# Performance work log

Measured on AMD Instinct MI355X. Metric: run time of the kernel, lower is better.

## Reference

```python
import jax, jax.numpy as jnp
import numpy as np

N, H, E, T, ED, AB = 50000, 64, 800000, 800000, 64, 16


def setup_inputs() -> dict:
    key = jax.random.key(0)
    ks = jax.random.split(key, 26)

    def nrm(k, shape, scale=1.0):
        return jax.random.normal(k, shape, dtype=jnp.float32) * scale

    d = {}
    d["s"] = nrm(ks[0], (N, H))
    d["v"] = nrm(ks[1], (N, H, 3))
    d["edge_index"] = jax.random.randint(ks[2], (2, E), 0, N, dtype=jnp.int32)
    d["edge_rbf"] = jax.random.uniform(ks[3], (E, ED), dtype=jnp.float32)
    raw_dir = jax.random.normal(ks[4], (E, 3), dtype=jnp.float32)
    d["edge_dir"] = raw_dir / jnp.linalg.norm(raw_dir, axis=-1, keepdims=True)
    d["triplet_kj"] = jax.random.randint(ks[5], (T,), 0, E, dtype=jnp.int32)
    d["triplet_ji"] = jax.random.randint(ks[6], (T,), 0, E, dtype=jnp.int32)
    d["angle_feat"] = jax.random.uniform(ks[7], (T, AB), dtype=jnp.float32)

    def lin(kw, kb, fan_in, fan_out):
        sc = 1.0 / np.sqrt(fan_in)
        return nrm(kw, (fan_in, fan_out), sc), nrm(kb, (fan_out,), sc)

    d["W_t1"], d["b_t1"] = lin(ks[8], ks[9], 2 * ED + AB, H)
    d["W_t2"], d["b_t2"] = lin(ks[10], ks[11], H, H)
    d["W_m1"], d["b_m1"] = lin(ks[12], ks[13], 2 * H + ED + H, H)
    d["W_m2"], d["b_m2"] = lin(ks[14], ks[15], H, 2 * H)
    d["W_u1"], d["b_u1"] = lin(ks[16], ks[17], 3 * H, H)
    d["W_u2"], d["b_u2"] = lin(ks[18], ks[19], H, H)
    d["W_g1"], d["b_g1"] = lin(ks[20], ks[21], 3 * H, H)
    d["W_g2"], d["b_g2"] = lin(ks[22], ks[23], H, H)
    d["ln_g"] = jnp.ones((H,), jnp.float32)
    d["ln_b"] = jnp.zeros((H,), jnp.float32)
    return d


def _mlp(x, W1, b1, W2, b2):
    return jax.nn.silu(x @ W1 + b1) @ W2 + b2


def reference(s, v, edge_index, edge_rbf, edge_dir, triplet_kj, triplet_ji,
              angle_feat, W_t1, b_t1, W_t2, b_t2, W_m1, b_m1, W_m2, b_m2,
              W_u1, b_u1, W_u2, b_u2, W_g1, b_g1, W_g2, b_g2, ln_g, ln_b):
    n_nodes, hid = s.shape
    n_edges = edge_rbf.shape[0]

    # 3-body triplet messages: gather two edge rbf rows + angle feature
    t_in = jnp.concatenate([edge_rbf[triplet_kj], edge_rbf[triplet_ji], angle_feat], axis=-1)
    t_msg = _mlp(t_in, W_t1, b_t1, W_t2, b_t2)                 # [T, H]
    angle_agg = jax.ops.segment_sum(t_msg, triplet_ji, num_segments=n_edges)  # [E, H]

    src, dst = edge_index[0], edge_index[1]
    msg_in = jnp.concatenate([s[src], s[dst], edge_rbf, angle_agg], axis=-1)  # [E, 4H]
    msg = _mlp(msg_in, W_m1, b_m1, W_m2, b_m2)                 # [E, 2H]
    m_s, m_v_coeff = jnp.split(msg, 2, axis=-1)

    agg_s = jax.ops.segment_sum(m_s, dst, num_segments=n_nodes)  # [N, H]
    m_v = m_v_coeff[:, :, None] * edge_dir[:, None, :]          # [E, H, 3]
    agg_v = jax.ops.segment_sum(m_v.reshape(n_edges, hid * 3), dst,
                                num_segments=n_nodes).reshape(n_nodes, hid, 3)

    v_norm = jnp.linalg.norm(v, axis=-1)                        # [N, H]
    ctx = jnp.concatenate([s, agg_s, v_norm], axis=-1)          # [N, 3H]
    s_new = s + _mlp(ctx, W_u1, b_u1, W_u2, b_u2)
    gate = jax.nn.sigmoid(_mlp(ctx, W_g1, b_g1, W_g2, b_g2))
    v_new = v + gate[..., None] * agg_v

    mu = s_new.mean(axis=-1, keepdims=True)
    var = s_new.var(axis=-1, keepdims=True)
    s_ln = (s_new - mu) / jnp.sqrt(var + 1e-5) * ln_g + ln_b
    s_out = jax.nn.silu(s_ln)
    return (s_out, v_new)
```

## Files before the change

kernel.cpp:

```cpp
#include <hip/hip_runtime.h>
#include <cstdint>
#include <cstddef>

#define NN 50000
#define NE 800000
#define NT 800000

typedef unsigned short u16;
typedef unsigned int u32;
typedef __attribute__((ext_vector_type(8))) short short8;
typedef __attribute__((ext_vector_type(4))) float f32x4;

__device__ __forceinline__ float silu_f(float x) { return x / (1.f + __expf(-x)); }
__device__ __forceinline__ float sigm_f(float x) { return 1.f / (1.f + __expf(-x)); }
__device__ __forceinline__ u16 f2b(float x) {
  u32 u = __float_as_uint(x);
  u32 r = u + 0x7fffu + ((u >> 16) & 1u);
  return (u16)(r >> 16);
}
__device__ __forceinline__ float b2f(u16 h) { return __uint_as_float(((u32)h) << 16); }

template <int RW>
__device__ __forceinline__ int lx(int r, int c) {
  return r * RW + ((((c >> 3) ^ (r & 7)) << 3) | (c & 7));
}

__global__ __launch_bounds__(256) void kcvt2(const float* __restrict__ erbf,
                                             u16* __restrict__ erbf_bf,
                                             const float* __restrict__ s,
                                             u16* __restrict__ s_bf) {
  int i = blockIdx.x * 256 + threadIdx.x;
  const float* in;
  u16* out;
  int j;
  if (i < NE * 16) { in = erbf; out = erbf_bf; j = i; }
  else { j = i - NE * 16; if (j >= NN * 16) return; in = s; out = s_bf; }
  float4 v = ((const float4*)in)[j];
  uint2 p;
  p.x = (u32)f2b(v.x) | ((u32)f2b(v.y) << 16);
  p.y = (u32)f2b(v.z) | ((u32)f2b(v.w) << 16);
  ((uint2*)out)[j] = p;
}

__global__ __launch_bounds__(256) void khist2(const int* __restrict__ tji,
                                              const int* __restrict__ edst,
                                              int* __restrict__ tcnt,
                                              int* __restrict__ ncnt) {
  int i = blockIdx.x * 256 + threadIdx.x;
  if (i < NT) atomicAdd(&tcnt[tji[i]], 1);
  else {
    int j = i - NT;
    if (j < NE) atomicAdd(&ncnt[edst[j]], 1);
  }
}

__global__ __launch_bounds__(256) void kscan1b(
    const int* __restrict__ inA, int nA, int* __restrict__ outA, int* __restrict__ bsA, int BA,
    const int* __restrict__ inB, int nB, int* __restrict__ outB, int* __restrict__ bsB) {
  __shared__ int sh[256];
  const int* in; int n; int* out; int* bs; int blk;
  if ((int)blockIdx.x < BA) { in = inA; n = nA; out = outA; bs = bsA; blk = blockIdx.x; }
  else { in = inB; n = nB; out = outB; bs = bsB; blk = blockIdx.x - BA; }
  int tid = threadIdx.x;
  size_t base = (size_t)blk * 1024;
  int v[4];
  int acc = 0;
#pragma unroll
  for (int q = 0; q < 4; ++q) {
    size_t i = base + (size_t)tid * 4 + q;
    int x = (i < (size_t)n) ? in[i] : 0;
    v[q] = acc;
    acc += x;
  }
  sh[tid] = acc;
  __syncthreads();
  for (int off = 1; off < 256; off <<= 1) {
    int y = (tid >= off) ? sh[tid - off] : 0;
    __syncthreads();
    sh[tid] += y;
    __syncthreads();
  }
  int excl = (tid == 0) ? 0 : sh[tid - 1];
  if (tid == 255) bs[blk] = sh[255];
#pragma unroll
  for (int q = 0; q < 4; ++q) {
    size_t i = base + (size_t)tid * 4 + q;
    if (i < (size_t)n) out[i] = excl + v[q];
  }
}

__global__ __launch_bounds__(1024) void kscan2b(int* __restrict__ bsA, int nbA,
                                                int* __restrict__ bsB, int nbB) {
  __shared__ int sh[1024];
  int* bs = (blockIdx.x == 0) ? bsA : bsB;
  int nb = (blockIdx.x == 0) ? nbA : nbB;
  int tid = threadIdx.x;
  sh[tid] = (tid < nb) ? bs[tid] : 0;
  __syncthreads();
  for (int off = 1; off < 1024; off <<= 1) {
    int y = (tid >= off) ? sh[tid - off] : 0;
    __syncthreads();
    sh[tid] += y;
    __syncthreads();
  }
  if (tid < nb) bs[tid] = (tid == 0) ? 0 : sh[tid - 1];
}

__global__ __launch_bounds__(256) void kscan3b(
    int* __restrict__ outA, const int* __restrict__ bsA, int nA, int totalA,
    int* __restrict__ outB, const int* __restrict__ bsB, int nB, int totalB) {
  int i = blockIdx.x * 256 + threadIdx.x;
  if (i <= nA) {
    if (i < nA) outA[i] += bsA[i >> 10];
    else outA[nA] = totalA;
  } else {
    int j = i - (nA + 1);
    if (j < nB) outB[j] += bsB[j >> 10];
    else if (j == nB) outB[nB] = totalB;
  }
}

__global__ __launch_bounds__(256) void kscatter_inv_afeat(
    const int* __restrict__ keys, const int* __restrict__ off, int n,
    int* __restrict__ cnt, int* __restrict__ tids,
    const float* __restrict__ afeat, u16* __restrict__ afeat_s) {
  int i = blockIdx.x * 256 + threadIdx.x;
  if (i < n) {
    int k = keys[i];
    int slot = off[k] + (atomicSub(&cnt[k], 1) - 1);
    tids[slot] = i;
    const float4* src = (const float4*)(afeat + (size_t)i * 16);
    uint2* dst = (uint2*)(afeat_s + (size_t)slot * 16);
#pragma unroll
    for (int q = 0; q < 4; ++q) {
      float4 v = src[q];
      uint2 p;
      p.x = (u32)f2b(v.x) | ((u32)f2b(v.y) << 16);
      p.y = (u32)f2b(v.z) | ((u32)f2b(v.w) << 16);
      dst[q] = p;
    }
  }
}

__global__ __launch_bounds__(256) void kscatter_fwd_dir(const int* __restrict__ keys,
                                                        const int* __restrict__ off, int n,
                                                        int* __restrict__ cnt,
                                                        int* __restrict__ eids,
                                                        const float* __restrict__ dir,
                                                        float* __restrict__ dir_s) {
  int i = blockIdx.x * 256 + threadIdx.x;
  if (i < n) {
    int k = keys[i];
    int slot = off[k] + (atomicSub(&cnt[k], 1) - 1);
    eids[slot] = i;
    dir_s[(size_t)slot * 3 + 0] = dir[(size_t)i * 3 + 0];
    dir_s[(size_t)slot * 3 + 1] = dir[(size_t)i * 3 + 1];
    dir_s[(size_t)slot * 3 + 2] = dir[(size_t)i * 3 + 2];
  }
}

__global__ __launch_bounds__(256) void kprepw_all(
    const float* __restrict__ Wt1, const float* __restrict__ Wt2,
    const float* __restrict__ Wm1, const float* __restrict__ Wm2,
    const float* __restrict__ Wu1, const float* __restrict__ Wu2,
    const float* __restrict__ Wg1, const float* __restrict__ Wg2,
    u16* __restrict__ Pt1, u16* __restrict__ Pt2,
    u16* __restrict__ Pm1, u16* __restrict__ Pm2,
    u16* __restrict__ Pu1, u16* __restrict__ Pu2,
    u16* __restrict__ Pg1, u16* __restrict__ Pg2) {
  int gid = blockIdx.x * 256 + threadIdx.x;
  int f = gid >> 6, l = gid & 63;
  const float* W; u16* out; int K, N, fl;
  if (f < 20)       { W = Wt1; out = Pt1; K = 144; N = 64;  fl = f; }
  else if (f < 28)  { W = Wt2; out = Pt2; K = 64;  N = 64;  fl = f - 20; }
  else if (f < 60)  { W = Wm1; out = Pm1; K = 256; N = 64;  fl = f - 28; }
  else if (f < 76)  { W = Wm2; out = Pm2; K = 64;  N = 128; fl = f - 60; }
  else if (f < 100) { W = Wu1; out = Pu1; K = 192; N = 64;  fl = f - 76; }
  else if (f < 108) { W = Wu2; out = Pu2; K = 64;  N = 64;  fl = f - 100; }
  else if (f < 132) { W = Wg1; out = Pg1; K = 192; N = 64;  fl = f - 108; }
  else if (f < 140) { W = Wg2; out = Pg2; K = 64;  N = 64;  fl = f - 132; }
  else return;
  int nt = fl % (N / 16);
  int kt = fl / (N / 16);
  int k0 = kt * 32 + (l >> 4) * 8;
  int n = nt * 16 + (l & 15);
  u16 vals[8];
#pragma unroll
  for (int j = 0; j < 8; ++j) {
    int kk = k0 + j;
    vals[j] = (kk < K) ? f2b(W[(size_t)kk * N + n]) : (u16)0;
  }
  uint4* dst = (uint4*)(out + (size_t)fl * 512 + l * 8);
  uint4 p;
  p.x = (u32)vals[0] | ((u32)vals[1] << 16);
  p.y = (u32)vals[2] | ((u32)vals[3] << 16);
  p.z = (u32)vals[4] | ((u32)vals[5] << 16);
  p.w = (u32)vals[6] | ((u32)vals[7] << 16);
  *dst = p;
}

__global__ __launch_bounds__(256) void ktrip_mfma(
    const int* __restrict__ tkj, const int* __restrict__ tji,
    const u16* __restrict__ erbf_bf, const u16* __restrict__ afeat_s,
    const int* __restrict__ tids,
    const u16* __restrict__ Wp1, const float* __restrict__ b1,
    const u16* __restrict__ Wp2, const float* __restrict__ b2,
    u16* __restrict__ tmsg_s) {
  __shared__ u16 Xs[64 * 192];
  __shared__ u16 Hs[64 * 64];
  const int tid = threadIdx.x;
  const int l = tid & 63;
  const int w = tid >> 6;
  const int st0 = blockIdx.x * 64;

#pragma unroll
  for (int it = 0; it < 4; ++it) {
    int idx = it * 256 + tid;
    int sel = idx >> 9, r = (idx >> 3) & 63, ch = idx & 7;
    int t = tids[st0 + r];
    int node = sel ? tji[t] : tkj[t];
    uint4 vv = *(const uint4*)&erbf_bf[(size_t)node * 64 + ch * 8];
    *(uint4*)&Xs[lx<192>(r, sel * 64 + ch * 8)] = vv;
  }
  {
    int r = tid >> 2, c = (tid & 3) * 4;
    uint2 p2 = *(const uint2*)&afeat_s[(size_t)(st0 + r) * 16 + c];
    *(uint2*)&Xs[lx<192>(r, 128 + c)] = p2;
  }
#pragma unroll
  for (int i = 0; i < 2; ++i) {
    int idx = i * 256 + tid;
    int r = idx >> 3, c = 144 + (idx & 7) * 2;
    *(u32*)&Xs[lx<192>(r, c)] = 0;
  }
  __syncthreads();

  f32x4 acc1[4];
  {
    float bias = b1[w * 16 + (l & 15)];
#pragma unroll
    for (int mt = 0; mt < 4; ++mt) acc1[mt] = (f32x4){bias, bias, bias, bias};
    for (int ks = 0; ks < 5; ++ks) {
      short8 bf = *(const short8*)(Wp1 + ((size_t)(ks * 4 + w) * 64 + l) * 8);
#pragma unroll
      for (int mt = 0; mt < 4; ++mt) {
        short8 af = *(const short8*)&Xs[lx<192>(mt * 16 + (l & 15), ks * 32 + ((l >> 4) << 3))];
        acc1[mt] = __builtin_amdgcn_mfma_f32_16x16x32_bf16(af, bf, acc1[mt], 0, 0, 0);
      }
    }
  }
#pragma unroll
  for (int mt = 0; mt < 4; ++mt)
#pragma unroll
    for (int q = 0; q < 4; ++q) {
      int r = mt * 16 + (l >> 4) * 4 + q;
      Hs[lx<64>(r, w * 16 + (l & 15))] = f2b(silu_f(acc1[mt][q]));
    }
  __syncthreads();

  f32x4 acc2[4];
  {
    float bias = b2[w * 16 + (l & 15)];
#pragma unroll
    for (int mt = 0; mt < 4; ++mt) acc2[mt] = (f32x4){bias, bias, bias, bias};
    for (int ks = 0; ks < 2; ++ks) {
      short8 bf = *(const short8*)(Wp2 + ((size_t)(ks * 4 + w) * 64 + l) * 8);
#pragma unroll
      for (int mt = 0; mt < 4; ++mt) {
        short8 af = *(const short8*)&Hs[lx<64>(mt * 16 + (l & 15), ks * 32 + ((l >> 4) << 3))];
        acc2[mt] = __builtin_amdgcn_mfma_f32_16x16x32_bf16(af, bf, acc2[mt], 0, 0, 0);
      }
    }
  }
  __syncthreads();
#pragma unroll
  for (int mt = 0; mt < 4; ++mt)
#pragma unroll
    for (int q = 0; q < 4; ++q) {
      int r = mt * 16 + (l >> 4) * 4 + q;
      Xs[lx<64>(r, w * 16 + (l & 15))] = f2b(acc2[mt][q]);
    }
  __syncthreads();
  for (int i = 0; i < 2; ++i) {
    int idx = i * 256 + tid;
    int r = idx >> 3, c0 = (idx & 7) << 3;
    uint4 val = *(const uint4*)&Xs[lx<64>(r, c0)];
    *(uint4*)(tmsg_s + (size_t)(st0 + r) * 64 + c0) = val;
  }
}

__global__ __launch_bounds__(256) void kmsg_mfma(
    const int* __restrict__ eidx, const u16* __restrict__ s_bf,
    const u16* __restrict__ erbf_bf,
    const int* __restrict__ toff, const u16* __restrict__ tmsg_s,
    const int* __restrict__ eids,
    const u16* __restrict__ Wp1, const float* __restrict__ b1,
    const u16* __restrict__ Wp2, const float* __restrict__ b2,
    u16* __restrict__ msg_s) {
  __shared__ u16 Xs[64 * 256];
  __shared__ u16 Hs[64 * 64];
  const int tid = threadIdx.x;
  const int l = tid & 63;
  const int w = tid >> 6;
  const int sl0 = blockIdx.x * 64;

#pragma unroll
  for (int i = 0; i < 2; ++i) {
    int idx = i * 256 + tid;
    int r = idx >> 3, c0 = (idx & 7) << 3;
    int e = eids[sl0 + r];
    uint4 vv = *(const uint4*)&erbf_bf[(size_t)e * 64 + c0];
    *(uint4*)&Xs[lx<256>(r, 128 + c0)] = vv;
  }
#pragma unroll
  for (int it = 0; it < 4; ++it) {
    int idx = it * 256 + tid;
    int sel = idx >> 9, r = (idx >> 3) & 63, ch = idx & 7;
    int e = eids[sl0 + r];
    int node = eidx[sel * NE + e];
    uint4 vv = *(const uint4*)&s_bf[(size_t)node * 64 + ch * 8];
    *(uint4*)&Xs[lx<256>(r, sel * 64 + ch * 8)] = vv;
  }
#pragma unroll
  for (int it = 0; it < 2; ++it) {
    int idx = it * 256 + tid;
    int r = idx >> 3, ch = idx & 7;
    int e = eids[sl0 + r];
    int r0 = toff[e], r1 = toff[e + 1];
    float a[8];
#pragma unroll
    for (int j = 0; j < 8; ++j) a[j] = 0.f;
    for (int ri = r0; ri < r1; ++ri) {
      uint4 pk = *(const uint4*)&tmsg_s[(size_t)ri * 64 + ch * 8];
      a[0] += b2f((u16)(pk.x & 0xffff)); a[1] += b2f((u16)(pk.x >> 16));
      a[2] += b2f((u16)(pk.y & 0xffff)); a[3] += b2f((u16)(pk.y >> 16));
      a[4] += b2f((u16)(pk.z & 0xffff)); a[5] += b2f((u16)(pk.z >> 16));
      a[6] += b2f((u16)(pk.w & 0xffff)); a[7] += b2f((u16)(pk.w >> 16));
    }
    uint4 p;
    p.x = (u32)f2b(a[0]) | ((u32)f2b(a[1]) << 16);
    p.y = (u32)f2b(a[2]) | ((u32)f2b(a[3]) << 16);
    p.z = (u32)f2b(a[4]) | ((u32)f2b(a[5]) << 16);
    p.w = (u32)f2b(a[6]) | ((u32)f2b(a[7]) << 16);
    *(uint4*)&Xs[lx<256>(r, 192 + ch * 8)] = p;
  }
  __syncthreads();

  f32x4 acc1[4];
  {
    float bias = b1[w * 16 + (l & 15)];
#pragma unroll
    for (int mt = 0; mt < 4; ++mt) acc1[mt] = (f32x4){bias, bias, bias, bias};
    for (int ks = 0; ks < 8; ++ks) {
      short8 bf = *(const short8*)(Wp1 + ((size_t)(ks * 4 + w) * 64 + l) * 8);
#pragma unroll
      for (int mt = 0; mt < 4; ++mt) {
        short8 af = *(const short8*)&Xs[lx<256>(mt * 16 + (l & 15), ks * 32 + ((l >> 4) << 3))];
        acc1[mt] = __builtin_amdgcn_mfma_f32_16x16x32_bf16(af, bf, acc1[mt], 0, 0, 0);
      }
    }
  }
#pragma unroll
  for (int mt = 0; mt < 4; ++mt)
#pragma unroll
    for (int q = 0; q < 4; ++q) {
      int r = mt * 16 + (l >> 4) * 4 + q;
      Hs[lx<64>(r, w * 16 + (l & 15))] = f2b(silu_f(acc1[mt][q]));
    }
  __syncthreads();

  f32x4 acc2[2][4];
#pragma unroll
  for (int pp = 0; pp < 2; ++pp) {
    int nt = w * 2 + pp;
    float bias = b2[nt * 16 + (l & 15)];
#pragma unroll
    for (int mt = 0; mt < 4; ++mt) acc2[pp][mt] = (f32x4){bias, bias, bias, bias};
    for (int ks = 0; ks < 2; ++ks) {
      short8 bf = *(const short8*)(Wp2 + ((size_t)(ks * 8 + nt) * 64 + l) * 8);
#pragma unroll
      for (int mt = 0; mt < 4; ++mt) {
        short8 af = *(const short8*)&Hs[lx<64>(mt * 16 + (l & 15), ks * 32 + ((l >> 4) << 3))];
        acc2[pp][mt] = __builtin_amdgcn_mfma_f32_16x16x32_bf16(af, bf, acc2[pp][mt], 0, 0, 0);
      }
    }
  }
  __syncthreads();
#pragma unroll
  for (int pp = 0; pp < 2; ++pp)
#pragma unroll
    for (int mt = 0; mt < 4; ++mt)
#pragma unroll
      for (int q = 0; q < 4; ++q) {
        int r = mt * 16 + (l >> 4) * 4 + q;
        Xs[lx<128>(r, (w * 2 + pp) * 16 + (l & 15))] = f2b(acc2[pp][mt][q]);
      }
  __syncthreads();
  for (int i = 0; i < 4; ++i) {
    int idx = i * 256 + tid;
    int r = idx >> 4, c0 = (idx & 15) << 3;
    uint4 val = *(const uint4*)&Xs[lx<128>(r, c0)];
    *(uint4*)(msg_s + (size_t)(sl0 + r) * 128 + c0) = val;
  }
}

__global__ __launch_bounds__(256) void kagg(
    const int* __restrict__ noff, const u16* __restrict__ msg_s,
    const float* __restrict__ dir_s,
    u16* __restrict__ aggs_bf, float* __restrict__ aggv) {
  const int lane = threadIdx.x & 63;
  const int wv = threadIdx.x >> 6;
  const int n = blockIdx.x * 4 + wv;
  if (n >= NN) return;
  const int r0 = noff[n], r1 = noff[n + 1];
  const int lrow = lane >> 4, lcol = lane & 15;
  const bool is_ms = (lcol < 8);

  float a[8];
  float v0[8], v1[8], v2[8];
#pragma unroll
  for (int j = 0; j < 8; ++j) { a[j] = 0.f; v0[j] = 0.f; v1[j] = 0.f; v2[j] = 0.f; }

  for (int r4 = r0; r4 < r1; r4 += 4) {
    int r = r4 + lrow;
    if (r < r1) {
      uint4 pk = *(const uint4*)&msg_s[(size_t)r * 128 + lcol * 8];
      float x[8];
      x[0] = b2f((u16)(pk.x & 0xffff)); x[1] = b2f((u16)(pk.x >> 16));
      x[2] = b2f((u16)(pk.y & 0xffff)); x[3] = b2f((u16)(pk.y >> 16));
      x[4] = b2f((u16)(pk.z & 0xffff)); x[5] = b2f((u16)(pk.z >> 16));
      x[6] = b2f((u16)(pk.w & 0xffff)); x[7] = b2f((u16)(pk.w >> 16));
      if (is_ms) {
#pragma unroll
        for (int j = 0; j < 8; ++j) a[j] += x[j];
      } else {
        float dx = dir_s[(size_t)r * 3 + 0];
        float dy = dir_s[(size_t)r * 3 + 1];
        float dz = dir_s[(size_t)r * 3 + 2];
#pragma unroll
        for (int j = 0; j < 8; ++j) {
          v0[j] += x[j] * dx; v1[j] += x[j] * dy; v2[j] += x[j] * dz;
        }
      }
    }
  }
#pragma unroll
  for (int j = 0; j < 8; ++j) {
    a[j] += __shfl_xor(a[j], 16);  a[j] += __shfl_xor(a[j], 32);
    v0[j] += __shfl_xor(v0[j], 16); v0[j] += __shfl_xor(v0[j], 32);
    v1[j] += __shfl_xor(v1[j], 16); v1[j] += __shfl_xor(v1[j], 32);
    v2[j] += __shfl_xor(v2[j], 16); v2[j] += __shfl_xor(v2[j], 32);
  }
  if (lrow == 0) {
    if (is_ms) {
      uint4 p;
      p.x = (u32)f2b(a[0]) | ((u32)f2b(a[1]) << 16);
      p.y = (u32)f2b(a[2]) | ((u32)f2b(a[3]) << 16);
      p.z = (u32)f2b(a[4]) | ((u32)f2b(a[5]) << 16);
      p.w = (u32)f2b(a[6]) | ((u32)f2b(a[7]) << 16);
      *(uint4*)&aggs_bf[(size_t)n * 64 + lcol * 8] = p;
    } else {
      int c0 = (lcol - 8) * 8;
      float* av = aggv + (size_t)n * 192 + (size_t)c0 * 3;
      float4 o0 = {v0[0], v1[0], v2[0], v0[1]};
      float4 o1 = {v1[1], v2[1], v0[2], v1[2]};
      float4 o2 = {v2[2], v0[3], v1[3], v2[3]};
      float4 o3 = {v0[4], v1[4], v2[4], v0[5]};
      float4 o4 = {v1[5], v2[5], v0[6], v1[6]};
      float4 o5 = {v2[6], v0[7], v1[7], v2[7]};
      float4* av4 = (float4*)av;
      av4[0] = o0; av4[1] = o1; av4[2] = o2; av4[3] = o3; av4[4] = o4; av4[5] = o5;
    }
  }
}

__global__ __launch_bounds__(256) void knode_mfma(
    const u16* __restrict__ s_bf, const float* __restrict__ v,
    const u16* __restrict__ aggs_bf, const float* __restrict__ aggv,
    const u16* __restrict__ WpU1, const float* __restrict__ bU1,
    const u16* __restrict__ WpU2, const float* __restrict__ bU2,
    const u16* __restrict__ WpG1, const float* __restrict__ bG1,
    const u16* __restrict__ WpG2, const float* __restrict__ bG2,
    const float* __restrict__ lng, const float* __restrict__ lnb,
    float* __restrict__ outs, float* __restrict__ outv) {
  __shared__ __align__(16) char smem[64 * 192 * 2 + 2 * 64 * 64 * 2];
  u16* Xs = (u16*)smem;
  u16* Hu = (u16*)(smem + 64 * 192 * 2);
  u16* Hg = Hu + 64 * 64;
  float* Fs = (float*)smem;

  const int tid = threadIdx.x;
  const int l = tid & 63;
  const int w = tid >> 6;
  const int n0 = blockIdx.x * 64;

  for (int i = 0; i < 2; ++i) {
    int idx = i * 256 + tid;
    int r = idx >> 3, c0 = (idx & 7) << 3;
    int nr = n0 + r; if (nr >= NN) nr = NN - 1;
    uint4 a = *(const uint4*)&s_bf[(size_t)nr * 64 + c0];
    *(uint4*)&Xs[lx<192>(r, c0)] = a;
    uint4 b = *(const uint4*)&aggs_bf[(size_t)nr * 64 + c0];
    *(uint4*)&Xs[lx<192>(r, 64 + c0)] = b;
  }
  for (int it = 0; it < 16; ++it) {
    int idx = it * 256 + tid;
    int r = idx >> 6, c = idx & 63;
    int nr = n0 + r; if (nr >= NN) nr = NN - 1;
    const float* vp = v + (size_t)nr * 192 + c * 3;
    float x = vp[0], y = vp[1], z = vp[2];
    Xs[lx<192>(r, 128 + c)] = f2b(sqrtf(x * x + y * y + z * z));
  }
  __syncthreads();

  f32x4 au[4], ag[4];
  {
    float biu = bU1[w * 16 + (l & 15)], big = bG1[w * 16 + (l & 15)];
#pragma unroll
    for (int mt = 0; mt < 4; ++mt) {
      au[mt] = (f32x4){biu, biu, biu, biu};
      ag[mt] = (f32x4){big, big, big, big};
    }
    for (int ks = 0; ks < 6; ++ks) {
      short8 bu = *(const short8*)(WpU1 + ((size_t)(ks * 4 + w) * 64 + l) * 8);
      short8 bg = *(const short8*)(WpG1 + ((size_t)(ks * 4 + w) * 64 + l) * 8);
#pragma unroll
      for (int mt = 0; mt < 4; ++mt) {
        short8 af = *(const short8*)&Xs[lx<192>(mt * 16 + (l & 15), ks * 32 + ((l >> 4) << 3))];
        au[mt] = __builtin_amdgcn_mfma_f32_16x16x32_bf16(af, bu, au[mt], 0, 0, 0);
        ag[mt] = __builtin_amdgcn_mfma_f32_16x16x32_bf16(af, bg, ag[mt], 0, 0, 0);
      }
    }
  }
#pragma unroll
  for (int mt = 0; mt < 4; ++mt)
#pragma unroll
    for (int q = 0; q < 4; ++q) {
      int r = mt * 16 + (l >> 4) * 4 + q;
      Hu[lx<64>(r, w * 16 + (l & 15))] = f2b(silu_f(au[mt][q]));
      Hg[lx<64>(r, w * 16 + (l & 15))] = f2b(silu_f(ag[mt][q]));
    }
  __syncthreads();

  f32x4 ou[4], og[4];
  {
    float biu = bU2[w * 16 + (l & 15)], big = bG2[w * 16 + (l & 15)];
#pragma unroll
    for (int mt = 0; mt < 4; ++mt) {
      ou[mt] = (f32x4){biu, biu, biu, biu};
      og[mt] = (f32x4){big, big, big, big};
    }
    for (int ks = 0; ks < 2; ++ks) {
      short8 bu = *(const short8*)(WpU2 + ((size_t)(ks * 4 + w) * 64 + l) * 8);
      short8 bg = *(const short8*)(WpG2 + ((size_t)(ks * 4 + w) * 64 + l) * 8);
#pragma unroll
      for (int mt = 0; mt < 4; ++mt) {
        short8 afu = *(const short8*)&Hu[lx<64>(mt * 16 + (l & 15), ks * 32 + ((l >> 4) << 3))];
        ou[mt] = __builtin_amdgcn_mfma_f32_16x16x32_bf16(afu, bu, ou[mt], 0, 0, 0);
        short8 afg = *(const short8*)&Hg[lx<64>(mt * 16 + (l & 15), ks * 32 + ((l >> 4) << 3))];
        og[mt] = __builtin_amdgcn_mfma_f32_16x16x32_bf16(afg, bg, og[mt], 0, 0, 0);
      }
    }
  }
#pragma unroll
  for (int mt = 0; mt < 4; ++mt)
#pragma unroll
    for (int q = 0; q < 4; ++q) {
      int r = mt * 16 + (l >> 4) * 4 + q;
      ou[mt][q] += b2f(Xs[lx<192>(r, w * 16 + (l & 15))]);
    }
  __syncthreads();

#pragma unroll
  for (int mt = 0; mt < 4; ++mt)
#pragma unroll
    for (int q = 0; q < 4; ++q) {
      int r = mt * 16 + (l >> 4) * 4 + q;
      Fs[r * 68 + w * 16 + (l & 15)] = ou[mt][q];
    }
  __syncthreads();
  {
    int r = tid >> 2, c0 = (tid & 3) * 16;
    float xv[16];
#pragma unroll
    for (int j4 = 0; j4 < 4; ++j4) {
      float4 t = *(const float4*)&Fs[r * 68 + c0 + j4 * 4];
      xv[j4 * 4 + 0] = t.x; xv[j4 * 4 + 1] = t.y;
      xv[j4 * 4 + 2] = t.z; xv[j4 * 4 + 3] = t.w;
    }
    float sm = 0.f, sq = 0.f;
#pragma unroll
    for (int j = 0; j < 16; ++j) { sm += xv[j]; sq += xv[j] * xv[j]; }
    sm += __shfl_xor(sm, 1); sq += __shfl_xor(sq, 1);
    sm += __shfl_xor(sm, 2); sq += __shfl_xor(sq, 2);
    float mu = sm * (1.f / 64.f);
    float var = sq * (1.f / 64.f) - mu * mu;
    float rstd = rsqrtf(var + 1e-5f);
    if (n0 + r < NN) {
      float* op = outs + (size_t)(n0 + r) * 64 + c0;
#pragma unroll
      for (int j4 = 0; j4 < 4; ++j4) {
        float4 o;
        float y0 = (xv[j4 * 4 + 0] - mu) * rstd * lng[c0 + j4 * 4 + 0] + lnb[c0 + j4 * 4 + 0];
        float y1 = (xv[j4 * 4 + 1] - mu) * rstd * lng[c0 + j4 * 4 + 1] + lnb[c0 + j4 * 4 + 1];
        float y2 = (xv[j4 * 4 + 2] - mu) * rstd * lng[c0 + j4 * 4 + 2] + lnb[c0 + j4 * 4 + 2];
        float y3 = (xv[j4 * 4 + 3] - mu) * rstd * lng[c0 + j4 * 4 + 3] + lnb[c0 + j4 * 4 + 3];
        o.x = silu_f(y0); o.y = silu_f(y1); o.z = silu_f(y2); o.w = silu_f(y3);
        *(float4*)(op + j4 * 4) = o;
      }
    }
  }
  __syncthreads();

#pragma unroll
  for (int mt = 0; mt < 4; ++mt)
#pragma unroll
    for (int q = 0; q < 4; ++q) {
      int r = mt * 16 + (l >> 4) * 4 + q;
      Fs[r * 68 + w * 16 + (l & 15)] = og[mt][q];
    }
  __syncthreads();
  {
    int r = tid >> 2, c0 = (tid & 3) * 16;
    int nr = n0 + r;
    if (nr < NN) {
      float gate[16];
#pragma unroll
      for (int j = 0; j < 16; ++j) gate[j] = sigm_f(Fs[r * 68 + c0 + j]);
      const float4* vp = (const float4*)(v + (size_t)nr * 192 + c0 * 3);
      const float4* ap = (const float4*)(aggv + (size_t)nr * 192 + c0 * 3);
      float4* op = (float4*)(outv + (size_t)nr * 192 + c0 * 3);
#pragma unroll
      for (int j4 = 0; j4 < 12; ++j4) {
        float4 vv = vp[j4], av = ap[j4], o;
        o.x = vv.x + gate[(j4 * 4 + 0) / 3] * av.x;
        o.y = vv.y + gate[(j4 * 4 + 1) / 3] * av.y;
        o.z = vv.z + gate[(j4 * 4 + 2) / 3] * av.z;
        o.w = vv.w + gate[(j4 * 4 + 3) / 3] * av.w;
        op[j4] = o;
      }
    }
  }
}

extern "C" void kernel_launch(void* const* d_in, const int* in_sizes, int n_in,
                              void* d_out, int out_size, void* d_ws, size_t ws_size,
                              hipStream_t stream) {
  const float* s     = (const float*)d_in[0];
  const float* v     = (const float*)d_in[1];
  const int*   eidx  = (const int*)d_in[2];
  const float* erbf  = (const float*)d_in[3];
  const float* edir  = (const float*)d_in[4];
  const int*   tkj   = (const int*)d_in[5];
  const int*   tji   = (const int*)d_in[6];
  const float* afeat = (const float*)d_in[7];
  const float* W_t1  = (const float*)d_in[8];
  const float* b_t1  = (const float*)d_in[9];
  const float* W_t2  = (const float*)d_in[10];
  const float* b_t2  = (const float*)d_in[11];
  const float* W_m1  = (const float*)d_in[12];
  const float* b_m1  = (const float*)d_in[13];
  const float* W_m2  = (const float*)d_in[14];
  const float* b_m2  = (const float*)d_in[15];
  const float* W_u1  = (const float*)d_in[16];
  const float* b_u1  = (const float*)d_in[17];
  const float* W_u2  = (const float*)d_in[18];
  const float* b_u2  = (const float*)d_in[19];
  const float* W_g1  = (const float*)d_in[20];
  const float* b_g1  = (const float*)d_in[21];
  const float* W_g2  = (const float*)d_in[22];
  const float* b_g2  = (const float*)d_in[23];
  const float* ln_g  = (const float*)d_in[24];
  const float* ln_b  = (const float*)d_in[25];

  char* w = (char*)d_ws;
  auto alloc = [&](size_t bytes) -> char* {
    char* p = w;
    w += (bytes + 255) & ~(size_t)255;
    return p;
  };
  int* toff  = (int*)alloc((size_t)(NE + 1) * 4);
  int* noff  = (int*)alloc((size_t)(NN + 1) * 4);
  int* tcnt  = (int*)alloc((size_t)NE * 4);
  int* ncnt  = (int*)alloc((size_t)NN * 4);
  int* tids  = (int*)alloc((size_t)NT * 4);
  int* eids  = (int*)alloc((size_t)NE * 4);
  int* bsum  = (int*)alloc(2048 * 4);
  float* dir_s = (float*)alloc((size_t)NE * 3 * 4);
  u16* msg_s  = (u16*)alloc((size_t)NE * 128 * 2);
  u16* tmsg_s = (u16*)alloc((size_t)NT * 64 * 2);
  u16* erbf_bf = (u16*)alloc((size_t)NE * 64 * 2);
  u16* s_bf    = (u16*)alloc((size_t)NN * 64 * 2);
  u16* Wp_t1 = (u16*)alloc((size_t)5 * 4 * 512 * 2);
  u16* Wp_t2 = (u16*)alloc((size_t)2 * 4 * 512 * 2);
  u16* Wp_m1 = (u16*)alloc((size_t)8 * 4 * 512 * 2);
  u16* Wp_m2 = (u16*)alloc((size_t)2 * 8 * 512 * 2);
  u16* Wp_u1 = (u16*)alloc((size_t)6 * 4 * 512 * 2);
  u16* Wp_u2 = (u16*)alloc((size_t)2 * 4 * 512 * 2);
  u16* Wp_g1 = (u16*)alloc((size_t)6 * 4 * 512 * 2);
  u16* Wp_g2 = (u16*)alloc((size_t)2 * 4 * 512 * 2);
  u16* afeat_s = msg_s;
  float* aggv = (float*)tmsg_s;
  u16* aggs_bf = tmsg_s + (size_t)NN * 384;

  hipMemsetAsync(tcnt, 0, (size_t)((char*)(ncnt + NN) - (char*)tcnt), stream);

  kcvt2<<<(NE * 16 + NN * 16 + 255) / 256, 256, 0, stream>>>(erbf, erbf_bf, s, s_bf);
  khist2<<<(NT + NE + 255) / 256, 256, 0, stream>>>(tji, eidx + NE, tcnt, ncnt);

  const int Bt = (NE + 1023) / 1024, Bn = (NN + 1023) / 1024;
  kscan1b<<<Bt + Bn, 256, 0, stream>>>(tcnt, NE, toff, bsum, Bt, ncnt, NN, noff, bsum + 1024);
  kscan2b<<<2, 1024, 0, stream>>>(bsum, Bt, bsum + 1024, Bn);
  kscan3b<<<(NE + 1 + NN + 1 + 255) / 256, 256, 0, stream>>>(toff, bsum, NE, NT,
                                                             noff, bsum + 1024, NN, NE);

  kscatter_inv_afeat<<<(NT + 255) / 256, 256, 0, stream>>>(tji, toff, NT, tcnt, tids,
                                                           afeat, afeat_s);
  kscatter_fwd_dir<<<(NE + 255) / 256, 256, 0, stream>>>(eidx + NE, noff, NE, ncnt, eids,
                                                         edir, dir_s);

  kprepw_all<<<35, 256, 0, stream>>>(W_t1, W_t2, W_m1, W_m2, W_u1, W_u2, W_g1, W_g2,
                                     Wp_t1, Wp_t2, Wp_m1, Wp_m2, Wp_u1, Wp_u2, Wp_g1, Wp_g2);

  ktrip_mfma<<<NT / 64, 256, 0, stream>>>(tkj, tji, erbf_bf, afeat_s, tids,
                                          Wp_t1, b_t1, Wp_t2, b_t2, tmsg_s);
  kmsg_mfma<<<NE / 64, 256, 0, stream>>>(eidx, s_bf, erbf_bf, toff, tmsg_s, eids,
                                         Wp_m1, b_m1, Wp_m2, b_m2, msg_s);
  kagg<<<(NN + 3) / 4, 256, 0, stream>>>(noff, msg_s, dir_s, aggs_bf, aggv);

  float* out_s = (float*)d_out;
  float* out_v = out_s + (size_t)NN * 64;
  knode_mfma<<<(NN + 63) / 64, 256, 0, stream>>>(s_bf, v, aggs_bf, aggv,
                                                 Wp_u1, b_u1, Wp_u2, b_u2,
                                                 Wp_g1, b_g1, Wp_g2, b_g2,
                                                 ln_g, ln_b, out_s, out_v);
}
```

Measured before the change: 643.5 us.

## Fuse node aggregation into message kernel epilogue and merge prep kernels

The per-node aggregation kernel is removed. The edge message MLP kernel now reduces its 64 dst-sorted rows in its epilogue, writing directly for segments contained in the tile and using float atomics for segments that cross tile boundaries. This avoids writing and re-reading the bf16 msg_s buffer of 800k by 128 values. The three prep kernels (two scatters and the weight packing) are merged into one launch, and the fp32 aggregation buffers are now zeroed by the memset. In exchange the epilogue runs a serial 64-row loop on only 128 threads, and atomic contention on boundary nodes makes the accumulation order nondeterministic.

```diff
diff --git a/kernel.cpp b/kernel.cpp
--- a/kernel.cpp
+++ b/kernel.cpp
@@ -19,6 +19,9 @@
   return (u16)(r >> 16);
 }
 __device__ __forceinline__ float b2f(u16 h) { return __uint_as_float(((u32)h) << 16); }
+__device__ __forceinline__ u32 pk2(float a, float b) {
+  return (u32)f2b(a) | ((u32)f2b(b) << 16);
+}
 
 template <int RW>
 __device__ __forceinline__ int lx(int r, int c) {
@@ -37,8 +40,8 @@
   else { j = i - NE * 16; if (j >= NN * 16) return; in = s; out = s_bf; }
   float4 v = ((const float4*)in)[j];
   uint2 p;
-  p.x = (u32)f2b(v.x) | ((u32)f2b(v.y) << 16);
-  p.y = (u32)f2b(v.z) | ((u32)f2b(v.w) << 16);
+  p.x = pk2(v.x, v.y);
+  p.y = pk2(v.z, v.w);
   ((uint2*)out)[j] = p;
 }
 
@@ -120,46 +123,11 @@
   }
 }
 
-__global__ __launch_bounds__(256) void kscatter_inv_afeat(
-    const int* __restrict__ keys, const int* __restrict__ off, int n,
-    int* __restrict__ cnt, int* __restrict__ tids,
-    const float* __restrict__ afeat, u16* __restrict__ afeat_s) {
-  int i = blockIdx.x * 256 + threadIdx.x;
-  if (i < n) {
-    int k = keys[i];
-    int slot = off[k] + (atomicSub(&cnt[k], 1) - 1);
-    tids[slot] = i;
-    const float4* src = (const float4*)(afeat + (size_t)i * 16);
-    uint2* dst = (uint2*)(afeat_s + (size_t)slot * 16);
-#pragma unroll
-    for (int q = 0; q < 4; ++q) {
-      float4 v = src[q];
-      uint2 p;
-      p.x = (u32)f2b(v.x) | ((u32)f2b(v.y) << 16);
-      p.y = (u32)f2b(v.z) | ((u32)f2b(v.w) << 16);
-      dst[q] = p;
-    }
-  }
-}
-
-__global__ __launch_bounds__(256) void kscatter_fwd_dir(const int* __restrict__ keys,
-                                                        const int* __restrict__ off, int n,
-                                                        int* __restrict__ cnt,
-                                                        int* __restrict__ eids,
-                                                        const float* __restrict__ dir,
-                                                        float* __restrict__ dir_s) {
-  int i = blockIdx.x * 256 + threadIdx.x;
-  if (i < n) {
-    int k = keys[i];
-    int slot = off[k] + (atomicSub(&cnt[k], 1) - 1);
-    eids[slot] = i;
-    dir_s[(size_t)slot * 3 + 0] = dir[(size_t)i * 3 + 0];
-    dir_s[(size_t)slot * 3 + 1] = dir[(size_t)i * 3 + 1];
-    dir_s[(size_t)slot * 3 + 2] = dir[(size_t)i * 3 + 2];
-  }
-}
-
-__global__ __launch_bounds__(256) void kprepw_all(
+__global__ __launch_bounds__(256) void kprep_all(
+    const int* __restrict__ tji, const int* __restrict__ toff, int* __restrict__ tcnt,
+    int* __restrict__ tids, const float* __restrict__ afeat, u16* __restrict__ afeat_s,
+    const int* __restrict__ edst, const int* __restrict__ noff, int* __restrict__ ncnt,
+    int* __restrict__ eids, const float* __restrict__ dir, float* __restrict__ dir_s,
     const float* __restrict__ Wt1, const float* __restrict__ Wt2,
     const float* __restrict__ Wm1, const float* __restrict__ Wm2,
     const float* __restrict__ Wu1, const float* __restrict__ Wu2,
@@ -168,35 +136,60 @@
     u16* __restrict__ Pm1, u16* __restrict__ Pm2,
     u16* __restrict__ Pu1, u16* __restrict__ Pu2,
     u16* __restrict__ Pg1, u16* __restrict__ Pg2) {
-  int gid = blockIdx.x * 256 + threadIdx.x;
-  int f = gid >> 6, l = gid & 63;
-  const float* W; u16* out; int K, N, fl;
-  if (f < 20)       { W = Wt1; out = Pt1; K = 144; N = 64;  fl = f; }
-  else if (f < 28)  { W = Wt2; out = Pt2; K = 64;  N = 64;  fl = f - 20; }
-  else if (f < 60)  { W = Wm1; out = Pm1; K = 256; N = 64;  fl = f - 28; }
-  else if (f < 76)  { W = Wm2; out = Pm2; K = 64;  N = 128; fl = f - 60; }
-  else if (f < 100) { W = Wu1; out = Pu1; K = 192; N = 64;  fl = f - 76; }
-  else if (f < 108) { W = Wu2; out = Pu2; K = 64;  N = 64;  fl = f - 100; }
-  else if (f < 132) { W = Wg1; out = Pg1; K = 192; N = 64;  fl = f - 108; }
-  else if (f < 140) { W = Wg2; out = Pg2; K = 64;  N = 64;  fl = f - 132; }
-  else return;
-  int nt = fl % (N / 16);
-  int kt = fl / (N / 16);
-  int k0 = kt * 32 + (l >> 4) * 8;
-  int n = nt * 16 + (l & 15);
-  u16 vals[8];
-#pragma unroll
-  for (int j = 0; j < 8; ++j) {
-    int kk = k0 + j;
-    vals[j] = (kk < K) ? f2b(W[(size_t)kk * N + n]) : (u16)0;
-  }
-  uint4* dst = (uint4*)(out + (size_t)fl * 512 + l * 8);
-  uint4 p;
-  p.x = (u32)vals[0] | ((u32)vals[1] << 16);
-  p.y = (u32)vals[2] | ((u32)vals[3] << 16);
-  p.z = (u32)vals[4] | ((u32)vals[5] << 16);
-  p.w = (u32)vals[6] | ((u32)vals[7] << 16);
-  *dst = p;
+  int i = blockIdx.x * 256 + threadIdx.x;
+  if (i < NT) {
+    int k = tji[i];
+    int slot = toff[k] + (atomicSub(&tcnt[k], 1) - 1);
+    tids[slot] = i;
+    const float4* src = (const float4*)(afeat + (size_t)i * 16);
+    uint2* dst = (uint2*)(afeat_s + (size_t)slot * 16);
+#pragma unroll
+    for (int q = 0; q < 4; ++q) {
+      float4 v = src[q];
+      uint2 p;
+      p.x = pk2(v.x, v.y);
+      p.y = pk2(v.z, v.w);
+      dst[q] = p;
+    }
+  } else if (i < NT + NE) {
+    int j = i - NT;
+    int k = edst[j];
+    int slot = noff[k] + (atomicSub(&ncnt[k], 1) - 1);
+    eids[slot] = j;
+    dir_s[(size_t)slot * 3 + 0] = dir[(size_t)j * 3 + 0];
+    dir_s[(size_t)slot * 3 + 1] = dir[(size_t)j * 3 + 1];
+    dir_s[(size_t)slot * 3 + 2] = dir[(size_t)j * 3 + 2];
+  } else {
+    int g = i - NT - NE;
+    int f = g >> 6, l = g & 63;
+    const float* W; u16* out; int K, N, fl;
+    if (f < 20)       { W = Wt1; out = Pt1; K = 144; N = 64;  fl = f; }
+    else if (f < 28)  { W = Wt2; out = Pt2; K = 64;  N = 64;  fl = f - 20; }
+    else if (f < 60)  { W = Wm1; out = Pm1; K = 256; N = 64;  fl = f - 28; }
+    else if (f < 76)  { W = Wm2; out = Pm2; K = 64;  N = 128; fl = f - 60; }
+    else if (f < 100) { W = Wu1; out = Pu1; K = 192; N = 64;  fl = f - 76; }
+    else if (f < 108) { W = Wu2; out = Pu2; K = 64;  N = 64;  fl = f - 100; }
+    else if (f < 132) { W = Wg1; out = Pg1; K = 192; N = 64;  fl = f - 108; }
+    else if (f < 140) { W = Wg2; out = Pg2; K = 64;  N = 64;  fl = f - 132; }
+    else return;
+    int nt = fl % (N / 16);
+    int kt = fl / (N / 16);
+    int k0 = kt * 32 + (l >> 4) * 8;
+    int n = nt * 16 + (l & 15);
+    u16 vals[8];
+#pragma unroll
+    for (int j = 0; j < 8; ++j) {
+      int kk = k0 + j;
+      vals[j] = (kk < K) ? f2b(W[(size_t)kk * N + n]) : (u16)0;
+    }
+    uint4* dst = (uint4*)(out + (size_t)fl * 512 + l * 8);
+    uint4 p;
+    p.x = (u32)vals[0] | ((u32)vals[1] << 16);
+    p.y = (u32)vals[2] | ((u32)vals[3] << 16);
+    p.z = (u32)vals[4] | ((u32)vals[5] << 16);
+    p.w = (u32)vals[6] | ((u32)vals[7] << 16);
+    *dst = p;
+  }
 }
 
 __global__ __launch_bounds__(256) void ktrip_mfma(
@@ -293,12 +286,16 @@
     const int* __restrict__ eidx, const u16* __restrict__ s_bf,
     const u16* __restrict__ erbf_bf,
     const int* __restrict__ toff, const u16* __restrict__ tmsg_s,
-    const int* __restrict__ eids,
+    const int* __restrict__ eids, const int* __restrict__ noff,
+    const float* __restrict__ dir_s,
     const u16* __restrict__ Wp1, const float* __restrict__ b1,
     const u16* __restrict__ Wp2, const float* __restrict__ b2,
-    u16* __restrict__ msg_s) {
-  __shared__ u16 Xs[64 * 256];
-  __shared__ u16 Hs[64 * 64];
+    float* __restrict__ aggs_f, float* __restrict__ aggv) {
+  __shared__ __align__(16) char smemM[64 * 256 * 2 + 64 * 64 * 2];
+  u16* Xs = (u16*)smemM;
+  u16* Hs = (u16*)(smemM + 64 * 256 * 2);
+  int* dstL = (int*)(smemM + 64 * 256 * 2);
+  float* dirL = (float*)(smemM + 64 * 256 * 2 + 256);
   const int tid = threadIdx.x;
   const int l = tid & 63;
   const int w = tid >> 6;
@@ -338,10 +335,10 @@
       a[6] += b2f((u16)(pk.w & 0xffff)); a[7] += b2f((u16)(pk.w >> 16));
     }
     uint4 p;
-    p.x = (u32)f2b(a[0]) | ((u32)f2b(a[1]) << 16);
-    p.y = (u32)f2b(a[2]) | ((u32)f2b(a[3]) << 16);
-    p.z = (u32)f2b(a[4]) | ((u32)f2b(a[5]) << 16);
-    p.w = (u32)f2b(a[6]) | ((u32)f2b(a[7]) << 16);
+    p.x = pk2(a[0], a[1]);
+    p.y = pk2(a[2], a[3]);
+    p.z = pk2(a[4], a[5]);
+    p.w = pk2(a[6], a[7]);
     *(uint4*)&Xs[lx<256>(r, 192 + ch * 8)] = p;
   }
   __syncthreads();
@@ -386,6 +383,7 @@
     }
   }
   __syncthreads();
+
 #pragma unroll
   for (int pp = 0; pp < 2; ++pp)
 #pragma unroll
@@ -395,88 +393,58 @@
         int r = mt * 16 + (l >> 4) * 4 + q;
         Xs[lx<128>(r, (w * 2 + pp) * 16 + (l & 15))] = f2b(acc2[pp][mt][q]);
       }
-  __syncthreads();
-  for (int i = 0; i < 4; ++i) {
-    int idx = i * 256 + tid;
-    int r = idx >> 4, c0 = (idx & 15) << 3;
-    uint4 val = *(const uint4*)&Xs[lx<128>(r, c0)];
-    *(uint4*)(msg_s + (size_t)(sl0 + r) * 128 + c0) = val;
-  }
-}
-
-__global__ __launch_bounds__(256) void kagg(
-    const int* __restrict__ noff, const u16* __restrict__ msg_s,
-    const float* __restrict__ dir_s,
-    u16* __restrict__ aggs_bf, float* __restrict__ aggv) {
-  const int lane = threadIdx.x & 63;
-  const int wv = threadIdx.x >> 6;
-  const int n = blockIdx.x * 4 + wv;
-  if (n >= NN) return;
-  const int r0 = noff[n], r1 = noff[n + 1];
-  const int lrow = lane >> 4, lcol = lane & 15;
-  const bool is_ms = (lcol < 8);
-
-  float a[8];
-  float v0[8], v1[8], v2[8];
-#pragma unroll
-  for (int j = 0; j < 8; ++j) { a[j] = 0.f; v0[j] = 0.f; v1[j] = 0.f; v2[j] = 0.f; }
-
-  for (int r4 = r0; r4 < r1; r4 += 4) {
-    int r = r4 + lrow;
-    if (r < r1) {
-      uint4 pk = *(const uint4*)&msg_s[(size_t)r * 128 + lcol * 8];
-      float x[8];
-      x[0] = b2f((u16)(pk.x & 0xffff)); x[1] = b2f((u16)(pk.x >> 16));
-      x[2] = b2f((u16)(pk.y & 0xffff)); x[3] = b2f((u16)(pk.y >> 16));
-      x[4] = b2f((u16)(pk.z & 0xffff)); x[5] = b2f((u16)(pk.z >> 16));
-      x[6] = b2f((u16)(pk.w & 0xffff)); x[7] = b2f((u16)(pk.w >> 16));
-      if (is_ms) {
-#pragma unroll
-        for (int j = 0; j < 8; ++j) a[j] += x[j];
-      } else {
-        float dx = dir_s[(size_t)r * 3 + 0];
-        float dy = dir_s[(size_t)r * 3 + 1];
-        float dz = dir_s[(size_t)r * 3 + 2];
-#pragma unroll
-        for (int j = 0; j < 8; ++j) {
-          v0[j] += x[j] * dx; v1[j] += x[j] * dy; v2[j] += x[j] * dz;
+  if (tid < 64) {
+    int e = eids[sl0 + tid];
+    dstL[tid] = eidx[NE + e];
+    dirL[tid * 3 + 0] = dir_s[(size_t)(sl0 + tid) * 3 + 0];
+    dirL[tid * 3 + 1] = dir_s[(size_t)(sl0 + tid) * 3 + 1];
+    dirL[tid * 3 + 2] = dir_s[(size_t)(sl0 + tid) * 3 + 2];
+  }
+  __syncthreads();
+
+  if (tid < 128) {
+    const int j = tid;
+    const bool ms = (j < 64);
+    float a0 = 0.f, a1 = 0.f, a2 = 0.f;
+    int cur = dstL[0];
+    for (int r = 0; r < 64; ++r) {
+      int d = dstL[r];
+      if (d != cur) {
+        bool interior = (noff[cur] >= sl0) && (noff[cur + 1] <= sl0 + 64);
+        if (ms) {
+          float* p = aggs_f + (size_t)cur * 64 + j;
+          if (interior) *p = a0; else atomicAdd(p, a0);
+        } else {
+          float* p = aggv + (size_t)cur * 192 + (size_t)(j - 64) * 3;
+          if (interior) { p[0] = a0; p[1] = a1; p[2] = a2; }
+          else { atomicAdd(p, a0); atomicAdd(p + 1, a1); atomicAdd(p + 2, a2); }
         }
-      }
-    }
-  }
-#pragma unroll
-  for (int j = 0; j < 8; ++j) {
-    a[j] += __shfl_xor(a[j], 16);  a[j] += __shfl_xor(a[j], 32);
-    v0[j] += __shfl_xor(v0[j], 16); v0[j] += __shfl_xor(v0[j], 32);
-    v1[j] += __shfl_xor(v1[j], 16); v1[j] += __shfl_xor(v1[j], 32);
-    v2[j] += __shfl_xor(v2[j], 16); v2[j] += __shfl_xor(v2[j], 32);
-  }
-  if (lrow == 0) {
-    if (is_ms) {
-      uint4 p;
-      p.x = (u32)f2b(a[0]) | ((u32)f2b(a[1]) << 16);
-      p.y = (u32)f2b(a[2]) | ((u32)f2b(a[3]) << 16);
-      p.z = (u32)f2b(a[4]) | ((u32)f2b(a[5]) << 16);
-      p.w = (u32)f2b(a[6]) | ((u32)f2b(a[7]) << 16);
-      *(uint4*)&aggs_bf[(size_t)n * 64 + lcol * 8] = p;
+        a0 = a1 = a2 = 0.f;
+        cur = d;
+      }
+      float val = b2f(Xs[lx<128>(r, j)]);
+      if (ms) a0 += val;
+      else {
+        a0 += val * dirL[r * 3 + 0];
+        a1 += val * dirL[r * 3 + 1];
+        a2 += val * dirL[r * 3 + 2];
+      }
+    }
+    bool interior = (noff[cur] >= sl0) && (noff[cur + 1] <= sl0 + 64);
+    if (ms) {
+      float* p = aggs_f + (size_t)cur * 64 + j;
+      if (interior) *p = a0; else atomicAdd(p, a0);
     } else {
-      int c0 = (lcol - 8) * 8;
-      float* av = aggv + (size_t)n * 192 + (size_t)c0 * 3;
-      float4 o0 = {v0[0], v1[0], v2[0], v0[1]};
-      float4 o1 = {v1[1], v2[1], v0[2], v1[2]};
-      float4 o2 = {v2[2], v0[3], v1[3], v2[3]};
-      float4 o3 = {v0[4], v1[4], v2[4], v0[5]};
-      float4 o4 = {v1[5], v2[5], v0[6], v1[6]};
-      float4 o5 = {v2[6], v0[7], v1[7], v2[7]};
-      float4* av4 = (float4*)av;
-      av4[0] = o0; av4[1] = o1; av4[2] = o2; av4[3] = o3; av4[4] = o4; av4[5] = o5;
+      float* p = aggv + (size_t)cur * 192 + (size_t)(j - 64) * 3;
+      if (interior) { p[0] = a0; p[1] = a1; p[2] = a2; }
+      else { atomicAdd(p, a0); atomicAdd(p + 1, a1); atomicAdd(p + 2, a2); }
     }
   }
 }
 
 __global__ __launch_bounds__(256) void knode_mfma(
     const u16* __restrict__ s_bf, const float* __restrict__ v,
-    const u16* __restrict__ aggs_bf, const float* __restrict__ aggv,
+    const float* __restrict__ aggs_f, const float* __restrict__ aggv,
     const u16* __restrict__ WpU1, const float* __restrict__ bU1,
     const u16* __restrict__ WpU2, const float* __restrict__ bU2,
     const u16* __restrict__ WpG1, const float* __restrict__ bG1,
@@ -500,7 +468,11 @@
     int nr = n0 + r; if (nr >= NN) nr = NN - 1;
     uint4 a = *(const uint4*)&s_bf[(size_t)nr * 64 + c0];
     *(uint4*)&Xs[lx<192>(r, c0)] = a;
-    uint4 b = *(const uint4*)&aggs_bf[(size_t)nr * 64 + c0];
+    const float4* ap = (const float4*)(aggs_f + (size_t)nr * 64 + c0);
+    float4 f0 = ap[0], f1 = ap[1];
+    uint4 b;
+    b.x = pk2(f0.x, f0.y); b.y = pk2(f0.z, f0.w);
+    b.z = pk2(f1.x, f1.y); b.w = pk2(f1.z, f1.w);
     *(uint4*)&Xs[lx<192>(r, 64 + c0)] = b;
   }
   for (int it = 0; it < 16; ++it) {
@@ -679,18 +651,22 @@
     w += (bytes + 255) & ~(size_t)255;
     return p;
   };
+  int* tcnt  = (int*)alloc((size_t)NE * 4);
+  int* ncnt  = (int*)alloc((size_t)NN * 4);
+  float* aggs_f = (float*)alloc((size_t)NN * 64 * 4);
+  float* aggv   = (float*)alloc((size_t)NN * 192 * 4);
+  size_t zspan = (size_t)((char*)(aggv + (size_t)NN * 192) - (char*)tcnt);
+
   int* toff  = (int*)alloc((size_t)(NE + 1) * 4);
   int* noff  = (int*)alloc((size_t)(NN + 1) * 4);
-  int* tcnt  = (int*)alloc((size_t)NE * 4);
-  int* ncnt  = (int*)alloc((size_t)NN * 4);
   int* tids  = (int*)alloc((size_t)NT * 4);
   int* eids  = (int*)alloc((size_t)NE * 4);
   int* bsum  = (int*)alloc(2048 * 4);
   float* dir_s = (float*)alloc((size_t)NE * 3 * 4);
-  u16* msg_s  = (u16*)alloc((size_t)NE * 128 * 2);
   u16* tmsg_s = (u16*)alloc((size_t)NT * 64 * 2);
   u16* erbf_bf = (u16*)alloc((size_t)NE * 64 * 2);
   u16* s_bf    = (u16*)alloc((size_t)NN * 64 * 2);
+  u16* afeat_s = (u16*)alloc((size_t)NT * 16 * 2);
   u16* Wp_t1 = (u16*)alloc((size_t)5 * 4 * 512 * 2);
   u16* Wp_t2 = (u16*)alloc((size_t)2 * 4 * 512 * 2);
   u16* Wp_m1 = (u16*)alloc((size_t)8 * 4 * 512 * 2);
@@ -699,11 +675,8 @@
   u16* Wp_u2 = (u16*)alloc((size_t)2 * 4 * 512 * 2);
   u16* Wp_g1 = (u16*)alloc((size_t)6 * 4 * 512 * 2);
   u16* Wp_g2 = (u16*)alloc((size_t)2 * 4 * 512 * 2);
-  u16* afeat_s = msg_s;
-  float* aggv = (float*)tmsg_s;
-  u16* aggs_bf = tmsg_s + (size_t)NN * 384;
-
-  hipMemsetAsync(tcnt, 0, (size_t)((char*)(ncnt + NN) - (char*)tcnt), stream);
+
+  hipMemsetAsync(tcnt, 0, zspan, stream);
 
   kcvt2<<<(NE * 16 + NN * 16 + 255) / 256, 256, 0, stream>>>(erbf, erbf_bf, s, s_bf);
   khist2<<<(NT + NE + 255) / 256, 256, 0, stream>>>(tji, eidx + NE, tcnt, ncnt);
@@ -714,23 +687,20 @@
   kscan3b<<<(NE + 1 + NN + 1 + 255) / 256, 256, 0, stream>>>(toff, bsum, NE, NT,
                                                              noff, bsum + 1024, NN, NE);
 
-  kscatter_inv_afeat<<<(NT + 255) / 256, 256, 0, stream>>>(tji, toff, NT, tcnt, tids,
-                                                           afeat, afeat_s);
-  kscatter_fwd_dir<<<(NE + 255) / 256, 256, 0, stream>>>(eidx + NE, noff, NE, ncnt, eids,
-                                                         edir, dir_s);
-
-  kprepw_all<<<35, 256, 0, stream>>>(W_t1, W_t2, W_m1, W_m2, W_u1, W_u2, W_g1, W_g2,
-                                     Wp_t1, Wp_t2, Wp_m1, Wp_m2, Wp_u1, Wp_u2, Wp_g1, Wp_g2);
+  kprep_all<<<(NT + NE + 140 * 64 + 255) / 256, 256, 0, stream>>>(
+      tji, toff, tcnt, tids, afeat, afeat_s,
+      eidx + NE, noff, ncnt, eids, edir, dir_s,
+      W_t1, W_t2, W_m1, W_m2, W_u1, W_u2, W_g1, W_g2,
+      Wp_t1, Wp_t2, Wp_m1, Wp_m2, Wp_u1, Wp_u2, Wp_g1, Wp_g2);
 
   ktrip_mfma<<<NT / 64, 256, 0, stream>>>(tkj, tji, erbf_bf, afeat_s, tids,
                                           Wp_t1, b_t1, Wp_t2, b_t2, tmsg_s);
-  kmsg_mfma<<<NE / 64, 256, 0, stream>>>(eidx, s_bf, erbf_bf, toff, tmsg_s, eids,
-                                         Wp_m1, b_m1, Wp_m2, b_m2, msg_s);
-  kagg<<<(NN + 3) / 4, 256, 0, stream>>>(noff, msg_s, dir_s, aggs_bf, aggv);
+  kmsg_mfma<<<NE / 64, 256, 0, stream>>>(eidx, s_bf, erbf_bf, toff, tmsg_s, eids, noff, dir_s,
+                                         Wp_m1, b_m1, Wp_m2, b_m2, aggs_f, aggv);
 
   float* out_s = (float*)d_out;
   float* out_v = out_s + (size_t)NN * 64;
-  knode_mfma<<<(NN + 63) / 64, 256, 0, stream>>>(s_bf, v, aggs_bf, aggv,
+  knode_mfma<<<(NN + 63) / 64, 256, 0, stream>>>(s_bf, v, aggs_f, aggv,
                                                  Wp_u1, b_u1, Wp_u2, b_u2,
                                                  Wp_g1, b_g1, Wp_g2, b_g2,
                                                  ln_g, ln_b, out_s, out_v);
```

Result: slower. 685.0 us (+6.4%).
